# Performance work log

Measured on AMD Instinct MI355X. Metric: run time of the kernel, lower is better.

The kernel has to match this reference:

```python
import jax, jax.numpy as jnp
import numpy as np

N_NODES = 100000
N_EDGES = 1600000
D_FEAT = 32


def setup_inputs() -> dict:
    key = jax.random.key(0)
    k1, k2, k3 = jax.random.split(key, 3)
    x = jax.random.normal(k1, (N_NODES, D_FEAT), dtype=jnp.float32)
    a = jax.random.randint(k2, (2, N_EDGES), 0, N_NODES, dtype=jnp.int64)
    e = jax.random.normal(k3, (N_EDGES,), dtype=jnp.float32)
    return {"x": x, "a": a, "e": e}


def reference(x, a, e):
    # phi: per-edge message = x[src] * e  (scalar edge weight)
    # sigma: per-target-node sum of incoming messages (0 for isolated nodes)
    src = a[0]
    tgt = a[1]
    msgs = x[src] * e[:, None]                       # [n_edges, d]
    out = jax.ops.segment_sum(msgs, tgt, num_segments=x.shape[0])  # [n_nodes, d]
    return out
```

## Files before the change

kernel.cpp:

```cpp
#include <hip/hip_runtime.h>
#include <hip/hip_bf16.h>


#define D_FEAT   32
#define SHIFT    7
#define BNODES   128
#define CHUNK    8192
#define MAXNB    1024
#define CAP      3072
#define ATHR     512
#define KMAX     (CAP / ATHR)

__device__ __forceinline__ unsigned short f2bf(float v) {
    union { float f; unsigned int u; } c; c.f = v;
    unsigned int r = c.u + 0x7FFFu + ((c.u >> 16) & 1u);
    return (unsigned short)(r >> 16);
}

__global__ void zero_out_kernel(float* __restrict__ out, int n) {
    int i = blockIdx.x * blockDim.x + threadIdx.x;
    if (i < n) out[i] = 0.0f;
}

__global__ void scatter_add_kernel(const float* __restrict__ x,
                                   const int* __restrict__ src,
                                   const int* __restrict__ tgt,
                                   const float* __restrict__ e,
                                   float* __restrict__ out,
                                   int n_edges) {
    long long gid   = (long long)blockIdx.x * blockDim.x + threadIdx.x;
    long long total = (long long)n_edges * D_FEAT;
    if (gid >= total) return;
    int edge = (int)(gid >> 5);
    int f    = (int)(gid & 31);
    float m = x[(long long)src[edge] * D_FEAT + f] * e[edge];
    atomicAdd(&out[(long long)tgt[edge] * D_FEAT + f], m);
}

__global__ void conv_bf16_kernel(const float* __restrict__ x,
                                 unsigned short* __restrict__ xh, int n) {
    int i = blockIdx.x * blockDim.x + threadIdx.x;
    int i4 = i << 2;
    if (i4 + 3 < n) {
        float4 v = ((const float4*)x)[i];
        ushort4 h;
        h.x = f2bf(v.x); h.y = f2bf(v.y); h.z = f2bf(v.z); h.w = f2bf(v.w);
        ((ushort4*)xh)[i] = h;
    } else {
        for (int j = i4; j < n; ++j) xh[j] = f2bf(x[j]);
    }
}


__global__ __launch_bounds__(1024) void p1_hist_kernel(
        const int* __restrict__ tgt, int* __restrict__ Hg,
        int n_edges, int NB, int nchunks) {
    __shared__ int cnt[MAXNB];
    for (int i = threadIdx.x; i < NB; i += 1024) cnt[i] = 0;
    __syncthreads();
    int base = blockIdx.x * CHUNK;
    int lim  = min(base + CHUNK, n_edges);
    int n    = lim - base;
    int nv   = n >> 2;
    const int4* t4p = (const int4*)(tgt + base);
    for (int v = threadIdx.x; v < nv; v += 1024) {
        int4 t4 = t4p[v];
        atomicAdd(&cnt[t4.x >> SHIFT], 1);
        atomicAdd(&cnt[t4.y >> SHIFT], 1);
        atomicAdd(&cnt[t4.z >> SHIFT], 1);
        atomicAdd(&cnt[t4.w >> SHIFT], 1);
    }
    for (int i = base + (nv << 2) + threadIdx.x; i < lim; i += 1024)
        atomicAdd(&cnt[tgt[i] >> SHIFT], 1);
    __syncthreads();
    for (int i = threadIdx.x; i < NB; i += 1024)
        Hg[i * nchunks + blockIdx.x] = cnt[i];
}

__global__ void scan_block_kernel(int* __restrict__ data, int* __restrict__ bsum,
                                  int n) {
    __shared__ int s[256];
    int i = blockIdx.x * 256 + threadIdx.x;
    int v = (i < n) ? data[i] : 0;
    s[threadIdx.x] = v;
    __syncthreads();
    #pragma unroll
    for (int d = 1; d < 256; d <<= 1) {
        int t = (threadIdx.x >= d) ? s[threadIdx.x - d] : 0;
        __syncthreads();
        s[threadIdx.x] += t;
        __syncthreads();
    }
    if (i < n) data[i] = s[threadIdx.x] - v;
    if (threadIdx.x == 255) bsum[blockIdx.x] = s[255];
}

__global__ void scan_bsum_kernel(int* __restrict__ bsum, int nblk) {
    __shared__ int s[1024];
    int tid = threadIdx.x;
    int v = (tid < nblk) ? bsum[tid] : 0;
    s[tid] = v;
    __syncthreads();
    for (int d = 1; d < 1024; d <<= 1) {
        int t = (tid >= d) ? s[tid - d] : 0;
        __syncthreads();
        s[tid] += t;
        __syncthreads();
    }
    if (tid < nblk) bsum[tid] = s[tid] - v;
}

__global__ __launch_bounds__(1024) void p1_scatter_kernel(
        const int* __restrict__ src,
        const int* __restrict__ tgt,
        const float* __restrict__ e,
        const int* __restrict__ Hg,
        const int* __restrict__ bsum,
        int2* __restrict__ rec,
        int n_edges, int NB, int nchunks) {
    __shared__ int cur[MAXNB];
    for (int i = threadIdx.x; i < NB; i += 1024) {
        int j = i * nchunks + blockIdx.x;
        cur[i] = Hg[j] + bsum[j >> 8];
    }
    __syncthreads();
    int base = blockIdx.x * CHUNK;
    int lim  = min(base + CHUNK, n_edges);
    int n    = lim - base;
    int nv   = n >> 2;
    const int4*   s4p = (const int4*)(src + base);
    const int4*   t4p = (const int4*)(tgt + base);
    const float4* e4p = (const float4*)(e + base);
    for (int v = threadIdx.x; v < nv; v += 1024) {
        int4   s4 = s4p[v];
        int4   t4 = t4p[v];
        float4 e4 = e4p[v];
        int p0 = atomicAdd(&cur[t4.x >> SHIFT], 1);
        int p1 = atomicAdd(&cur[t4.y >> SHIFT], 1);
        int p2 = atomicAdd(&cur[t4.z >> SHIFT], 1);
        int p3 = atomicAdd(&cur[t4.w >> SHIFT], 1);
        rec[p0] = make_int2(s4.x | ((t4.x & (BNODES - 1)) << 17), __float_as_int(e4.x));
        rec[p1] = make_int2(s4.y | ((t4.y & (BNODES - 1)) << 17), __float_as_int(e4.y));
        rec[p2] = make_int2(s4.z | ((t4.z & (BNODES - 1)) << 17), __float_as_int(e4.z));
        rec[p3] = make_int2(s4.w | ((t4.w & (BNODES - 1)) << 17), __float_as_int(e4.w));
    }
    for (int i = base + (nv << 2) + threadIdx.x; i < lim; i += 1024) {
        int t = tgt[i];
        int pos = atomicAdd(&cur[t >> SHIFT], 1);
        rec[pos] = make_int2(src[i] | ((t & (BNODES - 1)) << 17),
                             __float_as_int(e[i]));
    }
}

__global__ __launch_bounds__(ATHR) void p2_apply_bf16_kernel(
        const unsigned int* __restrict__ xhu,
        const int2* __restrict__ rec,
        const int* __restrict__ Hg, const int* __restrict__ bsum,
        float* __restrict__ out,
        int n_edges, int n_nodes, int NB, int nchunks) {
    __shared__ int2 srt[CAP];
    __shared__ unsigned short sidx[CAP];
    __shared__ int  cnt[BNODES];
    __shared__ int  off[BNODES + 1];
    __shared__ int  stmp[BNODES];

    int tid  = threadIdx.x;
    int b    = blockIdx.x;
    int j0   = b * nchunks;
    int base = Hg[j0] + bsum[j0 >> 8];
    int end;
    if (b + 1 < NB) {
        int j1 = (b + 1) * nchunks;
        end = Hg[j1] + bsum[j1 >> 8];
    } else {
        end = n_edges;
    }
    int nrec = end - base;

    if (nrec <= CAP) {
        if (tid < BNODES) cnt[tid] = 0;
        __syncthreads();
        int myln[KMAX];
        int myrk[KMAX];
        #pragma unroll
        for (int k = 0; k < KMAX; ++k) {
            int r = tid + k * ATHR;
            myln[k] = -1;
            if (r < nrec) {
                int2 a = rec[base + r];
                srt[r] = a;
                int ln = (a.x >> 17) & (BNODES - 1);
                myln[k] = ln;
                myrk[k] = atomicAdd(&cnt[ln], 1);
            }
        }
        __syncthreads();
        int v = (tid < BNODES) ? cnt[tid] : 0;
        if (tid < BNODES) stmp[tid] = v;
        __syncthreads();
        #pragma unroll
        for (int d = 1; d < BNODES; d <<= 1) {
            int t = (tid < BNODES && tid >= d) ? stmp[tid - d] : 0;
            __syncthreads();
            if (tid < BNODES) stmp[tid] += t;
            __syncthreads();
        }
        if (tid < BNODES) off[tid] = stmp[tid] - v;
        if (tid == 0) off[BNODES] = nrec;
        __syncthreads();
        #pragma unroll
        for (int k = 0; k < KMAX; ++k) {
            if (myln[k] >= 0)
                sidx[off[myln[k]] + myrk[k]] = (unsigned short)(tid + k * ATHR);
        }
        __syncthreads();
        int f2 = tid & 15;
        int g  = tid >> 4;
        for (int ln = g; ln < BNODES; ln += 32) {
            int p  = off[ln];
            int pe = off[ln + 1];
            float ax = 0.0f, ay = 0.0f;
            for (; p + 7 < pe; p += 8) {
                int2 r0 = srt[sidx[p]];
                int2 r1 = srt[sidx[p + 1]];
                int2 r2 = srt[sidx[p + 2]];
                int2 r3 = srt[sidx[p + 3]];
                int2 r4 = srt[sidx[p + 4]];
                int2 r5 = srt[sidx[p + 5]];
                int2 r6 = srt[sidx[p + 6]];
                int2 r7 = srt[sidx[p + 7]];
                unsigned int h0 = xhu[((r0.x & 0x1FFFF) << 4) + f2];
                unsigned int h1 = xhu[((r1.x & 0x1FFFF) << 4) + f2];
                unsigned int h2 = xhu[((r2.x & 0x1FFFF) << 4) + f2];
                unsigned int h3 = xhu[((r3.x & 0x1FFFF) << 4) + f2];
                unsigned int h4 = xhu[((r4.x & 0x1FFFF) << 4) + f2];
                unsigned int h5 = xhu[((r5.x & 0x1FFFF) << 4) + f2];
                unsigned int h6 = xhu[((r6.x & 0x1FFFF) << 4) + f2];
                unsigned int h7 = xhu[((r7.x & 0x1FFFF) << 4) + f2];
                float e0 = __int_as_float(r0.y), e1 = __int_as_float(r1.y);
                float e2 = __int_as_float(r2.y), e3 = __int_as_float(r3.y);
                float e4 = __int_as_float(r4.y), e5 = __int_as_float(r5.y);
                float e6 = __int_as_float(r6.y), e7 = __int_as_float(r7.y);
                ax += __uint_as_float(h0 << 16) * e0 + __uint_as_float(h1 << 16) * e1
                    + __uint_as_float(h2 << 16) * e2 + __uint_as_float(h3 << 16) * e3
                    + __uint_as_float(h4 << 16) * e4 + __uint_as_float(h5 << 16) * e5
                    + __uint_as_float(h6 << 16) * e6 + __uint_as_float(h7 << 16) * e7;
                ay += __uint_as_float(h0 & 0xFFFF0000u) * e0 + __uint_as_float(h1 & 0xFFFF0000u) * e1
                    + __uint_as_float(h2 & 0xFFFF0000u) * e2 + __uint_as_float(h3 & 0xFFFF0000u) * e3
                    + __uint_as_float(h4 & 0xFFFF0000u) * e4 + __uint_as_float(h5 & 0xFFFF0000u) * e5
                    + __uint_as_float(h6 & 0xFFFF0000u) * e6 + __uint_as_float(h7 & 0xFFFF0000u) * e7;
            }
            for (; p < pe; ++p) {
                int2 r0 = srt[sidx[p]];
                unsigned int h0 = xhu[((r0.x & 0x1FFFF) << 4) + f2];
                float e0 = __int_as_float(r0.y);
                ax += __uint_as_float(h0 << 16) * e0;
                ay += __uint_as_float(h0 & 0xFFFF0000u) * e0;
            }
            int node = (b << SHIFT) + ln;
            if (node < n_nodes) {
                float2 o; o.x = ax; o.y = ay;
                ((float2*)out)[node * (D_FEAT / 2) + f2] = o;
            }
        }
    } else {
        float* accS = (float*)srt;
        for (int i = tid; i < BNODES * D_FEAT; i += ATHR) accS[i] = 0.0f;
        __syncthreads();
        int f2 = tid & 15;
        for (int r = base + (tid >> 4); r < end; r += (ATHR >> 4)) {
            int2 a = rec[r];
            unsigned int h = xhu[((a.x & 0x1FFFF) << 4) + f2];
            float ev = __int_as_float(a.y);
            int ln = (a.x >> 17) & (BNODES - 1);
            atomicAdd(&accS[ln * D_FEAT + 2 * f2],     __uint_as_float(h << 16) * ev);
            atomicAdd(&accS[ln * D_FEAT + 2 * f2 + 1], __uint_as_float(h & 0xFFFF0000u) * ev);
        }
        __syncthreads();
        int out0 = b << SHIFT;
        for (int i = tid; i < BNODES * D_FEAT; i += ATHR) {
            int node = out0 + (i >> 5);
            if (node < n_nodes) out[(long long)out0 * D_FEAT + i] = accS[i];
        }
    }
}

__global__ __launch_bounds__(ATHR) void p2_apply_f32_kernel(
        const float* __restrict__ x, const int2* __restrict__ rec,
        const int* __restrict__ Hg, const int* __restrict__ bsum,
        float* __restrict__ out,
        int n_edges, int n_nodes, int NB, int nchunks) {
    __shared__ int2 srt[CAP];
    __shared__ unsigned short sidx[CAP];
    __shared__ int  cnt[BNODES];
    __shared__ int  off[BNODES + 1];
    __shared__ int  stmp[BNODES];

    int tid  = threadIdx.x;
    int b    = blockIdx.x;
    int j0   = b * nchunks;
    int base = Hg[j0] + bsum[j0 >> 8];
    int end;
    if (b + 1 < NB) {
        int j1 = (b + 1) * nchunks;
        end = Hg[j1] + bsum[j1 >> 8];
    } else {
        end = n_edges;
    }
    int nrec = end - base;

    if (nrec <= CAP) {
        if (tid < BNODES) cnt[tid] = 0;
        __syncthreads();
        int myln[KMAX];
        int myrk[KMAX];
        #pragma unroll
        for (int k = 0; k < KMAX; ++k) {
            int r = tid + k * ATHR;
            myln[k] = -1;
            if (r < nrec) {
                int2 a = rec[base + r];
                srt[r] = a;
                int ln = (a.x >> 17) & (BNODES - 1);
                myln[k] = ln;
                myrk[k] = atomicAdd(&cnt[ln], 1);
            }
        }
        __syncthreads();
        int v = (tid < BNODES) ? cnt[tid] : 0;
        if (tid < BNODES) stmp[tid] = v;
        __syncthreads();
        #pragma unroll
        for (int d = 1; d < BNODES; d <<= 1) {
            int t = (tid < BNODES && tid >= d) ? stmp[tid - d] : 0;
            __syncthreads();
            if (tid < BNODES) stmp[tid] += t;
            __syncthreads();
        }
        if (tid < BNODES) off[tid] = stmp[tid] - v;
        if (tid == 0) off[BNODES] = nrec;
        __syncthreads();
        #pragma unroll
        for (int k = 0; k < KMAX; ++k) {
            if (myln[k] >= 0)
                sidx[off[myln[k]] + myrk[k]] = (unsigned short)(tid + k * ATHR);
        }
        __syncthreads();
        int f = tid & 31;
        int g = tid >> 5;
        for (int ln = g; ln < BNODES; ln += 16) {
            int p  = off[ln];
            int pe = off[ln + 1];
            float acc = 0.0f;
            for (; p + 7 < pe; p += 8) {
                int2 r0 = srt[sidx[p]];
                int2 r1 = srt[sidx[p + 1]];
                int2 r2 = srt[sidx[p + 2]];
                int2 r3 = srt[sidx[p + 3]];
                int2 r4 = srt[sidx[p + 4]];
                int2 r5 = srt[sidx[p + 5]];
                int2 r6 = srt[sidx[p + 6]];
                int2 r7 = srt[sidx[p + 7]];
                float v0 = x[(r0.x & 0x1FFFF) * D_FEAT + f] * __int_as_float(r0.y);
                float v1 = x[(r1.x & 0x1FFFF) * D_FEAT + f] * __int_as_float(r1.y);
                float v2 = x[(r2.x & 0x1FFFF) * D_FEAT + f] * __int_as_float(r2.y);
                float v3 = x[(r3.x & 0x1FFFF) * D_FEAT + f] * __int_as_float(r3.y);
                float v4 = x[(r4.x & 0x1FFFF) * D_FEAT + f] * __int_as_float(r4.y);
                float v5 = x[(r5.x & 0x1FFFF) * D_FEAT + f] * __int_as_float(r5.y);
                float v6 = x[(r6.x & 0x1FFFF) * D_FEAT + f] * __int_as_float(r6.y);
                float v7 = x[(r7.x & 0x1FFFF) * D_FEAT + f] * __int_as_float(r7.y);
                acc += ((v0 + v1) + (v2 + v3)) + ((v4 + v5) + (v6 + v7));
            }
            for (; p < pe; ++p) {
                int2 r0 = srt[sidx[p]];
                acc += x[(r0.x & 0x1FFFF) * D_FEAT + f] * __int_as_float(r0.y);
            }
            int node = (b << SHIFT) + ln;
            if (node < n_nodes)
                out[(long long)node * D_FEAT + f] = acc;
        }
    } else {
        float* accS = (float*)srt;
        for (int i = tid; i < BNODES * D_FEAT; i += ATHR) accS[i] = 0.0f;
        __syncthreads();
        int f = tid & 31;
        for (int r = base + (tid >> 5); r < end; r += (ATHR >> 5)) {
            int2 a = rec[r];
            float v = x[(a.x & 0x1FFFF) * D_FEAT + f] * __int_as_float(a.y);
            atomicAdd(&accS[((a.x >> 17) & (BNODES - 1)) * D_FEAT + f], v);
        }
        __syncthreads();
        int out0 = b << SHIFT;
        for (int i = tid; i < BNODES * D_FEAT; i += ATHR) {
            int node = out0 + (i >> 5);
            if (node < n_nodes) out[(long long)out0 * D_FEAT + i] = accS[i];
        }
    }
}

extern "C" void kernel_launch(void* const* d_in, const int* in_sizes, int n_in,
                              void* d_out, int out_size, void* d_ws, size_t ws_size,
                              hipStream_t stream) {
    const float* x = (const float*)d_in[0];
    const int*   a = (const int*)d_in[1];
    const float* e = (const float*)d_in[2];

    int n_x     = in_sizes[0];
    int n_edges = in_sizes[2];
    int n_nodes = out_size / D_FEAT;
    const int* src = a;
    const int* tgt = a + n_edges;
    float* out = (float*)d_out;

    int NB        = (n_nodes + BNODES - 1) >> SHIFT;
    int nchunks   = (n_edges + CHUNK - 1) / CHUNK;
    int scan_n    = NB * nchunks;
    int nblk_scan = (scan_n + 255) / 256;

    size_t xh_bytes   = ((size_t)n_x * 2 + 15) & ~(size_t)15;
    size_t rec_bytes  = (size_t)n_edges * sizeof(int2);
    size_t hg_bytes   = (size_t)scan_n * sizeof(int);
    size_t bsum_bytes = (size_t)nblk_scan * sizeof(int);
    size_t need_f32   = rec_bytes + hg_bytes + bsum_bytes;
    size_t need_bf16  = xh_bytes + need_f32;

    bool shape_ok = (NB <= MAXNB) && (nblk_scan <= 1024) && (n_nodes <= (1 << 17));

    if (!shape_ok || ws_size < need_f32) {
        int threads = 256;
        zero_out_kernel<<<(out_size + threads - 1) / threads, threads, 0, stream>>>(out, out_size);
        long long total = (long long)n_edges * D_FEAT;
        int blocks = (int)((total + threads - 1) / threads);
        scatter_add_kernel<<<blocks, threads, 0, stream>>>(x, src, tgt, e, out, n_edges);
        return;
    }

    bool use_bf16 = (ws_size >= need_bf16);

    char* p = (char*)d_ws;
    unsigned short* xh = nullptr;
    if (use_bf16) { xh = (unsigned short*)p; p += xh_bytes; }
    int2* rec  = (int2*)p; p += rec_bytes;
    int*  Hg   = (int*)p;  p += hg_bytes;
    int*  bsum = (int*)p;

    if (use_bf16) {
        int cthreads = 256;
        int cblocks  = (n_x / 4 + cthreads - 1) / cthreads;
        conv_bf16_kernel<<<cblocks, cthreads, 0, stream>>>(x, xh, n_x);
    }

    p1_hist_kernel<<<nchunks, 1024, 0, stream>>>(tgt, Hg, n_edges, NB, nchunks);
    scan_block_kernel<<<nblk_scan, 256, 0, stream>>>(Hg, bsum, scan_n);
    scan_bsum_kernel<<<1, 1024, 0, stream>>>(bsum, nblk_scan);
    p1_scatter_kernel<<<nchunks, 1024, 0, stream>>>(src, tgt, e, Hg, bsum, rec, n_edges, NB, nchunks);
    if (use_bf16) {
        p2_apply_bf16_kernel<<<NB, ATHR, 0, stream>>>((const unsigned int*)xh, rec, Hg, bsum,
                                                      out, n_edges, n_nodes, NB, nchunks);
    } else {
        p2_apply_f32_kernel<<<NB, ATHR, 0, stream>>>(x, rec, Hg, bsum,
                                                     out, n_edges, n_nodes, NB, nchunks);
    }
}
```

Measured before the change: 65.05 us.

## Fuse bf16 conversion, histogram, scan and bucket scatter into one cooperative kernel

Replaces the five-launch first phase (bf16 conversion, histogram, two scans, scatter) with one cooperative-launch kernel that uses grid-wide syncs between stages. Chunk size becomes a runtime choice, picked so the grid fits one cooperative launch. The apply kernel now writes sorted records straight into shared memory instead of sorting through an index array, which removes an indirection per record. The intent is to cut launch and inter-kernel gaps. The cost is grid.sync overhead and fewer, larger chunks per block. The f32 fallback path is dropped, and the code now assumes the bf16 workspace fits.

```diff
diff --git a/kernel.cpp b/kernel.cpp
--- a/kernel.cpp
+++ b/kernel.cpp
@@ -1,11 +1,13 @@
 #include <hip/hip_runtime.h>
 #include <hip/hip_bf16.h>
+#include <hip/hip_cooperative_groups.h>
+
+namespace cg = cooperative_groups;
 
 
 #define D_FEAT   32
 #define SHIFT    7
 #define BNODES   128
-#define CHUNK    8192
 #define MAXNB    1024
 #define CAP      3072
 #define ATHR     512
@@ -51,15 +53,14 @@
     }
 }
 
-
 __global__ __launch_bounds__(1024) void p1_hist_kernel(
         const int* __restrict__ tgt, int* __restrict__ Hg,
-        int n_edges, int NB, int nchunks) {
+        int n_edges, int NB, int nchunks, int chunk) {
     __shared__ int cnt[MAXNB];
     for (int i = threadIdx.x; i < NB; i += 1024) cnt[i] = 0;
     __syncthreads();
-    int base = blockIdx.x * CHUNK;
-    int lim  = min(base + CHUNK, n_edges);
+    int base = blockIdx.x * chunk;
+    int lim  = min(base + chunk, n_edges);
     int n    = lim - base;
     int nv   = n >> 2;
     const int4* t4p = (const int4*)(tgt + base);
@@ -117,15 +118,15 @@
         const int* __restrict__ Hg,
         const int* __restrict__ bsum,
         int2* __restrict__ rec,
-        int n_edges, int NB, int nchunks) {
+        int n_edges, int NB, int nchunks, int chunk, int segshift) {
     __shared__ int cur[MAXNB];
     for (int i = threadIdx.x; i < NB; i += 1024) {
         int j = i * nchunks + blockIdx.x;
-        cur[i] = Hg[j] + bsum[j >> 8];
-    }
-    __syncthreads();
-    int base = blockIdx.x * CHUNK;
-    int lim  = min(base + CHUNK, n_edges);
+        cur[i] = Hg[j] + bsum[j >> segshift];
+    }
+    __syncthreads();
+    int base = blockIdx.x * chunk;
+    int lim  = min(base + chunk, n_edges);
     int n    = lim - base;
     int nv   = n >> 2;
     const int4*   s4p = (const int4*)(src + base);
@@ -152,14 +153,117 @@
     }
 }
 
+__global__ __launch_bounds__(1024) void p1_fused_kernel(
+        const float* __restrict__ x, unsigned short* __restrict__ xh, int n_x,
+        const int* __restrict__ src, const int* __restrict__ tgt,
+        const float* __restrict__ e,
+        int* __restrict__ Hg, int* __restrict__ bsum, int2* __restrict__ rec,
+        int n_edges, int NB, int nchunks, int scan_n, int chunk) {
+    cg::grid_group grid = cg::this_grid();
+    __shared__ int cnt[MAXNB];
+    __shared__ int sbuf[1024];
+    int tid = threadIdx.x, blk = blockIdx.x;
+
+    int n4 = n_x >> 2;
+    for (int i = blk * 1024 + tid; i < n4; i += nchunks * 1024) {
+        float4 v = ((const float4*)x)[i];
+        ushort4 h;
+        h.x = f2bf(v.x); h.y = f2bf(v.y); h.z = f2bf(v.z); h.w = f2bf(v.w);
+        ((ushort4*)xh)[i] = h;
+    }
+    if (blk == 0) {
+        for (int j = (n4 << 2) + tid; j < n_x; j += 1024) xh[j] = f2bf(x[j]);
+    }
+
+    for (int i = tid; i < NB; i += 1024) cnt[i] = 0;
+    __syncthreads();
+    int base = blk * chunk;
+    int lim  = min(base + chunk, n_edges);
+    int n    = max(lim - base, 0);
+    int nv   = n >> 2;
+    const int4* t4p = (const int4*)(tgt + base);
+    for (int v = tid; v < nv; v += 1024) {
+        int4 t4 = t4p[v];
+        atomicAdd(&cnt[t4.x >> SHIFT], 1);
+        atomicAdd(&cnt[t4.y >> SHIFT], 1);
+        atomicAdd(&cnt[t4.z >> SHIFT], 1);
+        atomicAdd(&cnt[t4.w >> SHIFT], 1);
+    }
+    for (int i = base + (nv << 2) + tid; i < lim; i += 1024)
+        atomicAdd(&cnt[tgt[i] >> SHIFT], 1);
+    __syncthreads();
+    for (int i = tid; i < NB; i += 1024)
+        Hg[i * nchunks + blk] = cnt[i];
+
+    grid.sync();
+
+    int nseg = (scan_n + 1023) >> 10;
+    for (int s = blk; s < nseg; s += nchunks) {
+        int i = (s << 10) + tid;
+        int v = (i < scan_n) ? Hg[i] : 0;
+        sbuf[tid] = v;
+        __syncthreads();
+        for (int d = 1; d < 1024; d <<= 1) {
+            int t = (tid >= d) ? sbuf[tid - d] : 0;
+            __syncthreads();
+            sbuf[tid] += t;
+            __syncthreads();
+        }
+        if (i < scan_n) Hg[i] = sbuf[tid] - v;
+        if (tid == 1023) bsum[s] = sbuf[1023];
+        __syncthreads();
+    }
+    grid.sync();
+
+    if (blk == 0) {
+        int v = (tid < nseg) ? bsum[tid] : 0;
+        sbuf[tid] = v;
+        __syncthreads();
+        for (int d = 1; d < 1024; d <<= 1) {
+            int t = (tid >= d) ? sbuf[tid - d] : 0;
+            __syncthreads();
+            sbuf[tid] += t;
+            __syncthreads();
+        }
+        if (tid < nseg) bsum[tid] = sbuf[tid] - v;
+    }
+    grid.sync();
+
+    for (int i = tid; i < NB; i += 1024) {
+        int j = i * nchunks + blk;
+        cnt[i] = Hg[j] + bsum[j >> 10];
+    }
+    __syncthreads();
+    const int4*   s4p = (const int4*)(src + base);
+    const float4* e4p = (const float4*)(e + base);
+    for (int v = tid; v < nv; v += 1024) {
+        int4   s4 = s4p[v];
+        int4   t4 = t4p[v];
+        float4 e4 = e4p[v];
+        int p0 = atomicAdd(&cnt[t4.x >> SHIFT], 1);
+        int p1 = atomicAdd(&cnt[t4.y >> SHIFT], 1);
+        int p2 = atomicAdd(&cnt[t4.z >> SHIFT], 1);
+        int p3 = atomicAdd(&cnt[t4.w >> SHIFT], 1);
+        rec[p0] = make_int2(s4.x | ((t4.x & (BNODES - 1)) << 17), __float_as_int(e4.x));
+        rec[p1] = make_int2(s4.y | ((t4.y & (BNODES - 1)) << 17), __float_as_int(e4.y));
+        rec[p2] = make_int2(s4.z | ((t4.z & (BNODES - 1)) << 17), __float_as_int(e4.z));
+        rec[p3] = make_int2(s4.w | ((t4.w & (BNODES - 1)) << 17), __float_as_int(e4.w));
+    }
+    for (int i = base + (nv << 2) + tid; i < lim; i += 1024) {
+        int t = tgt[i];
+        int pos = atomicAdd(&cnt[t >> SHIFT], 1);
+        rec[pos] = make_int2(src[i] | ((t & (BNODES - 1)) << 17),
+                             __float_as_int(e[i]));
+    }
+}
+
 __global__ __launch_bounds__(ATHR) void p2_apply_bf16_kernel(
         const unsigned int* __restrict__ xhu,
         const int2* __restrict__ rec,
         const int* __restrict__ Hg, const int* __restrict__ bsum,
         float* __restrict__ out,
-        int n_edges, int n_nodes, int NB, int nchunks) {
+        int n_edges, int n_nodes, int NB, int nchunks, int segshift) {
     __shared__ int2 srt[CAP];
-    __shared__ unsigned short sidx[CAP];
     __shared__ int  cnt[BNODES];
     __shared__ int  off[BNODES + 1];
     __shared__ int  stmp[BNODES];
@@ -167,11 +271,11 @@
     int tid  = threadIdx.x;
     int b    = blockIdx.x;
     int j0   = b * nchunks;
-    int base = Hg[j0] + bsum[j0 >> 8];
+    int base = Hg[j0] + bsum[j0 >> segshift];
     int end;
     if (b + 1 < NB) {
         int j1 = (b + 1) * nchunks;
-        end = Hg[j1] + bsum[j1 >> 8];
+        end = Hg[j1] + bsum[j1 >> segshift];
     } else {
         end = n_edges;
     }
@@ -180,15 +284,16 @@
     if (nrec <= CAP) {
         if (tid < BNODES) cnt[tid] = 0;
         __syncthreads();
-        int myln[KMAX];
-        int myrk[KMAX];
+        int2 myrec[KMAX];
+        int  myln[KMAX];
+        int  myrk[KMAX];
         #pragma unroll
         for (int k = 0; k < KMAX; ++k) {
             int r = tid + k * ATHR;
             myln[k] = -1;
             if (r < nrec) {
                 int2 a = rec[base + r];
-                srt[r] = a;
+                myrec[k] = a;
                 int ln = (a.x >> 17) & (BNODES - 1);
                 myln[k] = ln;
                 myrk[k] = atomicAdd(&cnt[ln], 1);
@@ -211,7 +316,7 @@
         #pragma unroll
         for (int k = 0; k < KMAX; ++k) {
             if (myln[k] >= 0)
-                sidx[off[myln[k]] + myrk[k]] = (unsigned short)(tid + k * ATHR);
+                srt[off[myln[k]] + myrk[k]] = myrec[k];
         }
         __syncthreads();
         int f2 = tid & 15;
@@ -221,14 +326,14 @@
             int pe = off[ln + 1];
             float ax = 0.0f, ay = 0.0f;
             for (; p + 7 < pe; p += 8) {
-                int2 r0 = srt[sidx[p]];
-                int2 r1 = srt[sidx[p + 1]];
-                int2 r2 = srt[sidx[p + 2]];
-                int2 r3 = srt[sidx[p + 3]];
-                int2 r4 = srt[sidx[p + 4]];
-                int2 r5 = srt[sidx[p + 5]];
-                int2 r6 = srt[sidx[p + 6]];
-                int2 r7 = srt[sidx[p + 7]];
+                int2 r0 = srt[p];
+                int2 r1 = srt[p + 1];
+                int2 r2 = srt[p + 2];
+                int2 r3 = srt[p + 3];
+                int2 r4 = srt[p + 4];
+                int2 r5 = srt[p + 5];
+                int2 r6 = srt[p + 6];
+                int2 r7 = srt[p + 7];
                 unsigned int h0 = xhu[((r0.x & 0x1FFFF) << 4) + f2];
                 unsigned int h1 = xhu[((r1.x & 0x1FFFF) << 4) + f2];
                 unsigned int h2 = xhu[((r2.x & 0x1FFFF) << 4) + f2];
@@ -251,7 +356,7 @@
                     + __uint_as_float(h6 & 0xFFFF0000u) * e6 + __uint_as_float(h7 & 0xFFFF0000u) * e7;
             }
             for (; p < pe; ++p) {
-                int2 r0 = srt[sidx[p]];
+                int2 r0 = srt[p];
                 unsigned int h0 = xhu[((r0.x & 0x1FFFF) << 4) + f2];
                 float e0 = __int_as_float(r0.y);
                 ax += __uint_as_float(h0 << 16) * e0;
@@ -285,119 +390,6 @@
     }
 }
 
-__global__ __launch_bounds__(ATHR) void p2_apply_f32_kernel(
-        const float* __restrict__ x, const int2* __restrict__ rec,
-        const int* __restrict__ Hg, const int* __restrict__ bsum,
-        float* __restrict__ out,
-        int n_edges, int n_nodes, int NB, int nchunks) {
-    __shared__ int2 srt[CAP];
-    __shared__ unsigned short sidx[CAP];
-    __shared__ int  cnt[BNODES];
-    __shared__ int  off[BNODES + 1];
-    __shared__ int  stmp[BNODES];
-
-    int tid  = threadIdx.x;
-    int b    = blockIdx.x;
-    int j0   = b * nchunks;
-    int base = Hg[j0] + bsum[j0 >> 8];
-    int end;
-    if (b + 1 < NB) {
-        int j1 = (b + 1) * nchunks;
-        end = Hg[j1] + bsum[j1 >> 8];
-    } else {
-        end = n_edges;
-    }
-    int nrec = end - base;
-
-    if (nrec <= CAP) {
-        if (tid < BNODES) cnt[tid] = 0;
-        __syncthreads();
-        int myln[KMAX];
-        int myrk[KMAX];
-        #pragma unroll
-        for (int k = 0; k < KMAX; ++k) {
-            int r = tid + k * ATHR;
-            myln[k] = -1;
-            if (r < nrec) {
-                int2 a = rec[base + r];
-                srt[r] = a;
-                int ln = (a.x >> 17) & (BNODES - 1);
-                myln[k] = ln;
-                myrk[k] = atomicAdd(&cnt[ln], 1);
-            }
-        }
-        __syncthreads();
-        int v = (tid < BNODES) ? cnt[tid] : 0;
-        if (tid < BNODES) stmp[tid] = v;
-        __syncthreads();
-        #pragma unroll
-        for (int d = 1; d < BNODES; d <<= 1) {
-            int t = (tid < BNODES && tid >= d) ? stmp[tid - d] : 0;
-            __syncthreads();
-            if (tid < BNODES) stmp[tid] += t;
-            __syncthreads();
-        }
-        if (tid < BNODES) off[tid] = stmp[tid] - v;
-        if (tid == 0) off[BNODES] = nrec;
-        __syncthreads();
-        #pragma unroll
-        for (int k = 0; k < KMAX; ++k) {
-            if (myln[k] >= 0)
-                sidx[off[myln[k]] + myrk[k]] = (unsigned short)(tid + k * ATHR);
-        }
-        __syncthreads();
-        int f = tid & 31;
-        int g = tid >> 5;
-        for (int ln = g; ln < BNODES; ln += 16) {
-            int p  = off[ln];
-            int pe = off[ln + 1];
-            float acc = 0.0f;
-            for (; p + 7 < pe; p += 8) {
-                int2 r0 = srt[sidx[p]];
-                int2 r1 = srt[sidx[p + 1]];
-                int2 r2 = srt[sidx[p + 2]];
-                int2 r3 = srt[sidx[p + 3]];
-                int2 r4 = srt[sidx[p + 4]];
-                int2 r5 = srt[sidx[p + 5]];
-                int2 r6 = srt[sidx[p + 6]];
-                int2 r7 = srt[sidx[p + 7]];
-                float v0 = x[(r0.x & 0x1FFFF) * D_FEAT + f] * __int_as_float(r0.y);
-                float v1 = x[(r1.x & 0x1FFFF) * D_FEAT + f] * __int_as_float(r1.y);
-                float v2 = x[(r2.x & 0x1FFFF) * D_FEAT + f] * __int_as_float(r2.y);
-                float v3 = x[(r3.x & 0x1FFFF) * D_FEAT + f] * __int_as_float(r3.y);
-                float v4 = x[(r4.x & 0x1FFFF) * D_FEAT + f] * __int_as_float(r4.y);
-                float v5 = x[(r5.x & 0x1FFFF) * D_FEAT + f] * __int_as_float(r5.y);
-                float v6 = x[(r6.x & 0x1FFFF) * D_FEAT + f] * __int_as_float(r6.y);
-                float v7 = x[(r7.x & 0x1FFFF) * D_FEAT + f] * __int_as_float(r7.y);
-                acc += ((v0 + v1) + (v2 + v3)) + ((v4 + v5) + (v6 + v7));
-            }
-            for (; p < pe; ++p) {
-                int2 r0 = srt[sidx[p]];
-                acc += x[(r0.x & 0x1FFFF) * D_FEAT + f] * __int_as_float(r0.y);
-            }
-            int node = (b << SHIFT) + ln;
-            if (node < n_nodes)
-                out[(long long)node * D_FEAT + f] = acc;
-        }
-    } else {
-        float* accS = (float*)srt;
-        for (int i = tid; i < BNODES * D_FEAT; i += ATHR) accS[i] = 0.0f;
-        __syncthreads();
-        int f = tid & 31;
-        for (int r = base + (tid >> 5); r < end; r += (ATHR >> 5)) {
-            int2 a = rec[r];
-            float v = x[(a.x & 0x1FFFF) * D_FEAT + f] * __int_as_float(a.y);
-            atomicAdd(&accS[((a.x >> 17) & (BNODES - 1)) * D_FEAT + f], v);
-        }
-        __syncthreads();
-        int out0 = b << SHIFT;
-        for (int i = tid; i < BNODES * D_FEAT; i += ATHR) {
-            int node = out0 + (i >> 5);
-            if (node < n_nodes) out[(long long)out0 * D_FEAT + i] = accS[i];
-        }
-    }
-}
-
 extern "C" void kernel_launch(void* const* d_in, const int* in_sizes, int n_in,
                               void* d_out, int out_size, void* d_ws, size_t ws_size,
                               hipStream_t stream) {
@@ -412,21 +404,36 @@
     const int* tgt = a + n_edges;
     float* out = (float*)d_out;
 
-    int NB        = (n_nodes + BNODES - 1) >> SHIFT;
-    int nchunks   = (n_edges + CHUNK - 1) / CHUNK;
-    int scan_n    = NB * nchunks;
-    int nblk_scan = (scan_n + 255) / 256;
-
-    size_t xh_bytes   = ((size_t)n_x * 2 + 15) & ~(size_t)15;
-    size_t rec_bytes  = (size_t)n_edges * sizeof(int2);
-    size_t hg_bytes   = (size_t)scan_n * sizeof(int);
-    size_t bsum_bytes = (size_t)nblk_scan * sizeof(int);
-    size_t need_f32   = rec_bytes + hg_bytes + bsum_bytes;
-    size_t need_bf16  = xh_bytes + need_f32;
-
-    bool shape_ok = (NB <= MAXNB) && (nblk_scan <= 1024) && (n_nodes <= (1 << 17));
-
-    if (!shape_ok || ws_size < need_f32) {
+    int NB = (n_nodes + BNODES - 1) >> SHIFT;
+
+    int coop = 0;
+    hipDeviceGetAttribute(&coop, hipDeviceAttributeCooperativeLaunch, 0);
+
+    const int cands[4] = {6272, 8192, 16384, 32768};
+    int chunk = 0, nchunks = 0, scan_n = 0;
+    size_t xh_bytes  = ((size_t)n_x * 2 + 15) & ~(size_t)15;
+    size_t rec_bytes = (size_t)n_edges * sizeof(int2);
+    size_t hg_bytes = 0, bsum_bytes = 0;
+    bool ok = false;
+    for (int ci = 0; ci < 4; ++ci) {
+        int c   = cands[ci];
+        int nc  = (n_edges + c - 1) / c;
+        int sn  = NB * nc;
+        int nb256 = (sn + 255) / 256;
+        size_t hb = (size_t)sn * sizeof(int);
+        size_t bb = (size_t)nb256 * sizeof(int);
+        bool shape = (NB <= MAXNB) && (n_nodes <= (1 << 17)) && (nb256 <= 1024);
+        bool coop_fit = (nc <= 256) && (((sn + 1023) >> 10) <= 1024);
+        if (!shape) continue;
+        if (coop && !coop_fit) continue;
+        if (ws_size >= xh_bytes + rec_bytes + hb + bb) {
+            chunk = c; nchunks = nc; scan_n = sn;
+            hg_bytes = hb; bsum_bytes = bb; ok = true;
+            break;
+        }
+    }
+
+    if (!ok) {
         int threads = 256;
         zero_out_kernel<<<(out_size + threads - 1) / threads, threads, 0, stream>>>(out, out_size);
         long long total = (long long)n_edges * D_FEAT;
@@ -435,30 +442,35 @@
         return;
     }
 
-    bool use_bf16 = (ws_size >= need_bf16);
-
     char* p = (char*)d_ws;
-    unsigned short* xh = nullptr;
-    if (use_bf16) { xh = (unsigned short*)p; p += xh_bytes; }
+    unsigned short* xh = (unsigned short*)p; p += xh_bytes;
     int2* rec  = (int2*)p; p += rec_bytes;
     int*  Hg   = (int*)p;  p += hg_bytes;
     int*  bsum = (int*)p;
 
-    if (use_bf16) {
+    if (coop) {
+        void* args[] = { (void*)&x, (void*)&xh, (void*)&n_x,
+                         (void*)&src, (void*)&tgt, (void*)&e,
+                         (void*)&Hg, (void*)&bsum, (void*)&rec,
+                         (void*)&n_edges, (void*)&NB, (void*)&nchunks,
+                         (void*)&scan_n, (void*)&chunk };
+        hipLaunchCooperativeKernel((void*)p1_fused_kernel, dim3(nchunks),
+                                   dim3(1024), args, 0, stream);
+        p2_apply_bf16_kernel<<<NB, ATHR, 0, stream>>>(
+            (const unsigned int*)xh, rec, Hg, bsum, out,
+            n_edges, n_nodes, NB, nchunks, 10);
+    } else {
+        int nblk_scan = (scan_n + 255) / 256;
         int cthreads = 256;
         int cblocks  = (n_x / 4 + cthreads - 1) / cthreads;
         conv_bf16_kernel<<<cblocks, cthreads, 0, stream>>>(x, xh, n_x);
-    }
-
-    p1_hist_kernel<<<nchunks, 1024, 0, stream>>>(tgt, Hg, n_edges, NB, nchunks);
-    scan_block_kernel<<<nblk_scan, 256, 0, stream>>>(Hg, bsum, scan_n);
-    scan_bsum_kernel<<<1, 1024, 0, stream>>>(bsum, nblk_scan);
-    p1_scatter_kernel<<<nchunks, 1024, 0, stream>>>(src, tgt, e, Hg, bsum, rec, n_edges, NB, nchunks);
-    if (use_bf16) {
-        p2_apply_bf16_kernel<<<NB, ATHR, 0, stream>>>((const unsigned int*)xh, rec, Hg, bsum,
-                                                      out, n_edges, n_nodes, NB, nchunks);
-    } else {
-        p2_apply_f32_kernel<<<NB, ATHR, 0, stream>>>(x, rec, Hg, bsum,
-                                                     out, n_edges, n_nodes, NB, nchunks);
-    }
-}
+        p1_hist_kernel<<<nchunks, 1024, 0, stream>>>(tgt, Hg, n_edges, NB, nchunks, chunk);
+        scan_block_kernel<<<nblk_scan, 256, 0, stream>>>(Hg, bsum, scan_n);
+        scan_bsum_kernel<<<1, 1024, 0, stream>>>(bsum, nblk_scan);
+        p1_scatter_kernel<<<nchunks, 1024, 0, stream>>>(src, tgt, e, Hg, bsum, rec,
+                                                        n_edges, NB, nchunks, chunk, 8);
+        p2_apply_bf16_kernel<<<NB, ATHR, 0, stream>>>(
+            (const unsigned int*)xh, rec, Hg, bsum, out,
+            n_edges, n_nodes, NB, nchunks, 8);
+    }
+}
```

Result: slower. 159.9 us (+145.8%).

## Fuse bf16 conversion into histogram kernel and sort records directly in LDS

Applied to the files above, without the earlier changes.

The separate fp32-to-bf16 conversion kernel is removed and its work folded into the histogram kernel with a grid-stride loop, saving one kernel launch. In the apply kernels, records are kept in registers and scattered straight into their sorted position in shared memory, which drops the sidx index array and the double indirection in the gather loop. In exchange, register pressure rises from the extra int2 per slot, and the histogram kernel now also carries the conversion's memory traffic.

```diff
diff --git a/kernel.cpp b/kernel.cpp
--- a/kernel.cpp
+++ b/kernel.cpp
@@ -37,24 +37,24 @@
     atomicAdd(&out[(long long)tgt[edge] * D_FEAT + f], m);
 }
 
-__global__ void conv_bf16_kernel(const float* __restrict__ x,
-                                 unsigned short* __restrict__ xh, int n) {
-    int i = blockIdx.x * blockDim.x + threadIdx.x;
-    int i4 = i << 2;
-    if (i4 + 3 < n) {
-        float4 v = ((const float4*)x)[i];
-        ushort4 h;
-        h.x = f2bf(v.x); h.y = f2bf(v.y); h.z = f2bf(v.z); h.w = f2bf(v.w);
-        ((ushort4*)xh)[i] = h;
-    } else {
-        for (int j = i4; j < n; ++j) xh[j] = f2bf(x[j]);
-    }
-}
-
 
 __global__ __launch_bounds__(1024) void p1_hist_kernel(
+        const float* __restrict__ x, unsigned short* __restrict__ xh, int n_x,
         const int* __restrict__ tgt, int* __restrict__ Hg,
         int n_edges, int NB, int nchunks) {
+    if (xh) {
+        int n4 = n_x >> 2;
+        for (int i = blockIdx.x * 1024 + threadIdx.x; i < n4; i += nchunks * 1024) {
+            float4 v = ((const float4*)x)[i];
+            ushort4 h;
+            h.x = f2bf(v.x); h.y = f2bf(v.y); h.z = f2bf(v.z); h.w = f2bf(v.w);
+            ((ushort4*)xh)[i] = h;
+        }
+        if (blockIdx.x == 0) {
+            for (int j = (n4 << 2) + threadIdx.x; j < n_x; j += 1024)
+                xh[j] = f2bf(x[j]);
+        }
+    }
     __shared__ int cnt[MAXNB];
     for (int i = threadIdx.x; i < NB; i += 1024) cnt[i] = 0;
     __syncthreads();
@@ -159,7 +159,6 @@
         float* __restrict__ out,
         int n_edges, int n_nodes, int NB, int nchunks) {
     __shared__ int2 srt[CAP];
-    __shared__ unsigned short sidx[CAP];
     __shared__ int  cnt[BNODES];
     __shared__ int  off[BNODES + 1];
     __shared__ int  stmp[BNODES];
@@ -180,15 +179,16 @@
     if (nrec <= CAP) {
         if (tid < BNODES) cnt[tid] = 0;
         __syncthreads();
-        int myln[KMAX];
-        int myrk[KMAX];
+        int2 myrec[KMAX];
+        int  myln[KMAX];
+        int  myrk[KMAX];
         #pragma unroll
         for (int k = 0; k < KMAX; ++k) {
             int r = tid + k * ATHR;
             myln[k] = -1;
             if (r < nrec) {
                 int2 a = rec[base + r];
-                srt[r] = a;
+                myrec[k] = a;
                 int ln = (a.x >> 17) & (BNODES - 1);
                 myln[k] = ln;
                 myrk[k] = atomicAdd(&cnt[ln], 1);
@@ -211,7 +211,7 @@
         #pragma unroll
         for (int k = 0; k < KMAX; ++k) {
             if (myln[k] >= 0)
-                sidx[off[myln[k]] + myrk[k]] = (unsigned short)(tid + k * ATHR);
+                srt[off[myln[k]] + myrk[k]] = myrec[k];
         }
         __syncthreads();
         int f2 = tid & 15;
@@ -221,14 +221,14 @@
             int pe = off[ln + 1];
             float ax = 0.0f, ay = 0.0f;
             for (; p + 7 < pe; p += 8) {
-                int2 r0 = srt[sidx[p]];
-                int2 r1 = srt[sidx[p + 1]];
-                int2 r2 = srt[sidx[p + 2]];
-                int2 r3 = srt[sidx[p + 3]];
-                int2 r4 = srt[sidx[p + 4]];
-                int2 r5 = srt[sidx[p + 5]];
-                int2 r6 = srt[sidx[p + 6]];
-                int2 r7 = srt[sidx[p + 7]];
+                int2 r0 = srt[p];
+                int2 r1 = srt[p + 1];
+                int2 r2 = srt[p + 2];
+                int2 r3 = srt[p + 3];
+                int2 r4 = srt[p + 4];
+                int2 r5 = srt[p + 5];
+                int2 r6 = srt[p + 6];
+                int2 r7 = srt[p + 7];
                 unsigned int h0 = xhu[((r0.x & 0x1FFFF) << 4) + f2];
                 unsigned int h1 = xhu[((r1.x & 0x1FFFF) << 4) + f2];
                 unsigned int h2 = xhu[((r2.x & 0x1FFFF) << 4) + f2];
@@ -251,7 +251,7 @@
                     + __uint_as_float(h6 & 0xFFFF0000u) * e6 + __uint_as_float(h7 & 0xFFFF0000u) * e7;
             }
             for (; p < pe; ++p) {
-                int2 r0 = srt[sidx[p]];
+                int2 r0 = srt[p];
                 unsigned int h0 = xhu[((r0.x & 0x1FFFF) << 4) + f2];
                 float e0 = __int_as_float(r0.y);
                 ax += __uint_as_float(h0 << 16) * e0;
@@ -291,7 +291,6 @@
         float* __restrict__ out,
         int n_edges, int n_nodes, int NB, int nchunks) {
     __shared__ int2 srt[CAP];
-    __shared__ unsigned short sidx[CAP];
     __shared__ int  cnt[BNODES];
     __shared__ int  off[BNODES + 1];
     __shared__ int  stmp[BNODES];
@@ -312,15 +311,16 @@
     if (nrec <= CAP) {
         if (tid < BNODES) cnt[tid] = 0;
         __syncthreads();
-        int myln[KMAX];
-        int myrk[KMAX];
+        int2 myrec[KMAX];
+        int  myln[KMAX];
+        int  myrk[KMAX];
         #pragma unroll
         for (int k = 0; k < KMAX; ++k) {
             int r = tid + k * ATHR;
             myln[k] = -1;
             if (r < nrec) {
                 int2 a = rec[base + r];
-                srt[r] = a;
+                myrec[k] = a;
                 int ln = (a.x >> 17) & (BNODES - 1);
                 myln[k] = ln;
                 myrk[k] = atomicAdd(&cnt[ln], 1);
@@ -343,7 +343,7 @@
         #pragma unroll
         for (int k = 0; k < KMAX; ++k) {
             if (myln[k] >= 0)
-                sidx[off[myln[k]] + myrk[k]] = (unsigned short)(tid + k * ATHR);
+                srt[off[myln[k]] + myrk[k]] = myrec[k];
         }
         __syncthreads();
         int f = tid & 31;
@@ -353,14 +353,14 @@
             int pe = off[ln + 1];
             float acc = 0.0f;
             for (; p + 7 < pe; p += 8) {
-                int2 r0 = srt[sidx[p]];
-                int2 r1 = srt[sidx[p + 1]];
-                int2 r2 = srt[sidx[p + 2]];
-                int2 r3 = srt[sidx[p + 3]];
-                int2 r4 = srt[sidx[p + 4]];
-                int2 r5 = srt[sidx[p + 5]];
-                int2 r6 = srt[sidx[p + 6]];
-                int2 r7 = srt[sidx[p + 7]];
+                int2 r0 = srt[p];
+                int2 r1 = srt[p + 1];
+                int2 r2 = srt[p + 2];
+                int2 r3 = srt[p + 3];
+                int2 r4 = srt[p + 4];
+                int2 r5 = srt[p + 5];
+                int2 r6 = srt[p + 6];
+                int2 r7 = srt[p + 7];
                 float v0 = x[(r0.x & 0x1FFFF) * D_FEAT + f] * __int_as_float(r0.y);
                 float v1 = x[(r1.x & 0x1FFFF) * D_FEAT + f] * __int_as_float(r1.y);
                 float v2 = x[(r2.x & 0x1FFFF) * D_FEAT + f] * __int_as_float(r2.y);
@@ -372,7 +372,7 @@
                 acc += ((v0 + v1) + (v2 + v3)) + ((v4 + v5) + (v6 + v7));
             }
             for (; p < pe; ++p) {
-                int2 r0 = srt[sidx[p]];
+                int2 r0 = srt[p];
                 acc += x[(r0.x & 0x1FFFF) * D_FEAT + f] * __int_as_float(r0.y);
             }
             int node = (b << SHIFT) + ln;
@@ -444,21 +444,18 @@
     int*  Hg   = (int*)p;  p += hg_bytes;
     int*  bsum = (int*)p;
 
-    if (use_bf16) {
-        int cthreads = 256;
-        int cblocks  = (n_x / 4 + cthreads - 1) / cthreads;
-        conv_bf16_kernel<<<cblocks, cthreads, 0, stream>>>(x, xh, n_x);
-    }
-
-    p1_hist_kernel<<<nchunks, 1024, 0, stream>>>(tgt, Hg, n_edges, NB, nchunks);
+    p1_hist_kernel<<<nchunks, 1024, 0, stream>>>(x, xh, n_x, tgt, Hg,
+                                                 n_edges, NB, nchunks);
     scan_block_kernel<<<nblk_scan, 256, 0, stream>>>(Hg, bsum, scan_n);
     scan_bsum_kernel<<<1, 1024, 0, stream>>>(bsum, nblk_scan);
-    p1_scatter_kernel<<<nchunks, 1024, 0, stream>>>(src, tgt, e, Hg, bsum, rec, n_edges, NB, nchunks);
+    p1_scatter_kernel<<<nchunks, 1024, 0, stream>>>(src, tgt, e, Hg, bsum, rec,
+                                                    n_edges, NB, nchunks);
     if (use_bf16) {
-        p2_apply_bf16_kernel<<<NB, ATHR, 0, stream>>>((const unsigned int*)xh, rec, Hg, bsum,
-                                                      out, n_edges, n_nodes, NB, nchunks);
+        p2_apply_bf16_kernel<<<NB, ATHR, 0, stream>>>(
+            (const unsigned int*)xh, rec, Hg, bsum, out,
+            n_edges, n_nodes, NB, nchunks);
     } else {
-        p2_apply_f32_kernel<<<NB, ATHR, 0, stream>>>(x, rec, Hg, bsum,
-                                                     out, n_edges, n_nodes, NB, nchunks);
-    }
-}
+        p2_apply_f32_kernel<<<NB, ATHR, 0, stream>>>(
+            x, rec, Hg, bsum, out, n_edges, n_nodes, NB, nchunks);
+    }
+}
```

After: 58.14 us, median of 2. 1.12x faster.
